# Optimization experiments

Measured on AMD Instinct MI355X. Metric: run time of the kernel, lower is better.

Reference implementation:

```python
import jax, jax.numpy as jnp
import numpy as np

N, E, G = 50000, 400000, 64          # nodes, edges, graphs in batch
IN_DIM, OUT_DIM = 64, 128
N_ETYPES, N_STEPS = 4, 8


def setup_inputs() -> dict:
    key = jax.random.key(0)
    ks = jax.random.split(key, 13)
    s = 1.0 / np.sqrt(OUT_DIM)
    u = lambda k, shp: jax.random.uniform(k, shp, jnp.float32, -s, s)
    return {
        "node_features": jax.random.normal(ks[0], (N, IN_DIM), jnp.float32),
        "src": jax.random.randint(ks[1], (E,), 0, N),
        "dst": jax.random.randint(ks[2], (E,), 0, N),
        "etype": jax.random.randint(ks[3], (E,), 0, N_ETYPES),
        "graph_ids": jax.random.randint(ks[4], (N,), 0, G),
        "Ws": u(ks[5], (N_ETYPES, OUT_DIM, OUT_DIM)),   # per-edge-type linear
        "bs": u(ks[6], (N_ETYPES, OUT_DIM)),
        "W_ih": u(ks[7], (3 * OUT_DIM, OUT_DIM)),        # GRUCell (r,z,n order)
        "W_hh": u(ks[8], (3 * OUT_DIM, OUT_DIM)),
        "b_ih": u(ks[9], (3 * OUT_DIM,)),
        "b_hh": u(ks[10], (3 * OUT_DIM,)),
        "W_cls": u(ks[11], (1, OUT_DIM + IN_DIM)),
        "b_cls": u(ks[12], (1,)),
    }


def _gru_cell(x, h, W_ih, W_hh, b_ih, b_hh):
    gi = x @ W_ih.T + b_ih
    gh = h @ W_hh.T + b_hh
    ir, iz, i_n = jnp.split(gi, 3, axis=-1)
    hr, hz, h_n = jnp.split(gh, 3, axis=-1)
    r = jax.nn.sigmoid(ir + hr)
    z = jax.nn.sigmoid(iz + hz)
    n = jnp.tanh(i_n + r * h_n)
    return (1.0 - z) * n + z * h


def reference(node_features, src, dst, etype, graph_ids,
              Ws, bs, W_ih, W_hh, b_ih, b_hh, W_cls, b_cls):
    # pad input features to OUT_DIM (GGNN.forward zero_pad)
    h = jnp.concatenate(
        [node_features, jnp.zeros((N, OUT_DIM - IN_DIM), node_features.dtype)], -1)

    def step(h, _):
        # per-edge-type linear transform of all node states: (T, N, D)
        Wh = jnp.einsum('nd,tkd->tnk', h, Ws) + bs[:, None, :]
        msg = Wh[etype, src]                                  # (E, D) gather
        a = jax.ops.segment_sum(msg, dst, num_segments=N)     # scatter-add
        return _gru_cell(a, h, W_ih, W_hh, b_ih, b_hh), None

    h, _ = jax.lax.scan(step, h, None, length=N_STEPS)

    hcat = jnp.concatenate([h, node_features], -1)            # (N, OUT+IN)
    feats = jax.ops.segment_sum(hcat, graph_ids, num_segments=G)  # sum readout
    return jax.nn.sigmoid(feats @ W_cls.T + b_cls)            # (G, 1)
```

## Files before the change

### kernel.cpp

```cpp
#include <hip/hip_runtime.h>
#include <hip/hip_bf16.h>
#include <math.h>


#define NN 50000
#define NE 400000
#define NG 64
#define IND 64
#define OD 128
#define LDO 896
#define RC 8

typedef _Float16 f16x8 __attribute__((ext_vector_type(8)));
typedef _Float16 f16x4 __attribute__((ext_vector_type(4)));
typedef _Float16 f16x2 __attribute__((ext_vector_type(2)));
typedef float f32x4 __attribute__((ext_vector_type(4)));

__device__ inline unsigned short f2h(float x) {
    _Float16 hv = (_Float16)x;
    unsigned short u;
    __builtin_memcpy(&u, &hv, 2);
    return u;
}

__global__ void k_cvt(const float* __restrict__ s, unsigned short* __restrict__ d, int n) {
    int i = blockIdx.x * 256 + threadIdx.x;
    if (i < n) d[i] = f2h(s[i]);
}

__global__ void k_init_h(const float* __restrict__ nf, float* __restrict__ h,
                         unsigned short* __restrict__ hb) {
    int i = blockIdx.x * 256 + threadIdx.x;
    if (i >= NN * OD) return;
    int n = i >> 7, d = i & 127;
    float v = (d < IND) ? nf[n * IND + d] : 0.f;
    h[i] = v;
    hb[i] = f2h(v);
}

__global__ void k_count(const int* __restrict__ dst, int* __restrict__ deg) {
    int e = blockIdx.x * 256 + threadIdx.x;
    if (e < NE) atomicAdd(&deg[dst[e]], 1);
}

__global__ void k_scan1(const int* __restrict__ deg, int* __restrict__ rowp,
                        int* __restrict__ bsum) {
    __shared__ int buf[1024];
    int tid = threadIdx.x;
    int i = blockIdx.x * 1024 + tid;
    int v = (i < NN) ? deg[i] : 0;
    buf[tid] = v;
    __syncthreads();
    for (int off = 1; off < 1024; off <<= 1) {
        int t = (tid >= off) ? buf[tid - off] : 0;
        __syncthreads();
        buf[tid] += t;
        __syncthreads();
    }
    if (i < NN) rowp[i + 1] = buf[tid];
    if (tid == 1023) bsum[blockIdx.x] = buf[tid];
}

__global__ void k_scan2(int* __restrict__ bsum, int nb) {
    __shared__ int buf[64];
    int tid = threadIdx.x;
    int v = (tid < nb) ? bsum[tid] : 0;
    buf[tid] = v;
    __syncthreads();
    for (int off = 1; off < 64; off <<= 1) {
        int t = (tid >= off) ? buf[tid - off] : 0;
        __syncthreads();
        buf[tid] += t;
        __syncthreads();
    }
    if (tid < nb) bsum[tid] = buf[tid] - v;
}

__global__ void k_scan3(const int* __restrict__ deg, const int* __restrict__ bsum,
                        int* __restrict__ rowp, int* __restrict__ cursor) {
    int i = blockIdx.x * 256 + threadIdx.x;
    if (i >= NN) return;
    int incl = rowp[i + 1] + bsum[i >> 10];
    rowp[i + 1] = incl;
    cursor[i] = incl - deg[i];
    if (i == 0) rowp[0] = 0;
}

__global__ void k_fill(const int* __restrict__ src, const int* __restrict__ dst,
                       const int* __restrict__ et, int* __restrict__ cursor,
                       int* __restrict__ ebase) {
    int e = blockIdx.x * 256 + threadIdx.x;
    if (e < NE) {
        int pos = atomicAdd(&cursor[dst[e]], 1);
        ebase[pos] = src[e] * LDO + et[e] * 128;
    }
}

__global__ void k_gcount(const int* __restrict__ gid, int* __restrict__ gdeg) {
    __shared__ int c[NG];
    int tid = threadIdx.x;
    if (tid < NG) c[tid] = 0;
    __syncthreads();
    int n = blockIdx.x * 1024 + tid;
    if (n < NN) atomicAdd(&c[gid[n]], 1);
    __syncthreads();
    if (tid < NG && c[tid] > 0) atomicAdd(&gdeg[tid], c[tid]);
}

__global__ void k_gscan(const int* __restrict__ gdeg, int* __restrict__ growp,
                        int* __restrict__ gcur) {
    __shared__ int buf[NG];
    int tid = threadIdx.x;
    int v = gdeg[tid];
    buf[tid] = v;
    __syncthreads();
    for (int off = 1; off < NG; off <<= 1) {
        int t = (tid >= off) ? buf[tid - off] : 0;
        __syncthreads();
        buf[tid] += t;
        __syncthreads();
    }
    growp[tid + 1] = buf[tid];
    gcur[tid] = buf[tid] - v;
    if (tid == 0) growp[0] = 0;
}

__global__ void k_gfill(const int* __restrict__ gid, int* __restrict__ gcur,
                        int* __restrict__ nlist) {
    __shared__ int lcnt[NG];
    __shared__ int lbase[NG];
    int tid = threadIdx.x;
    if (tid < NG) lcnt[tid] = 0;
    __syncthreads();
    int n = blockIdx.x * 1024 + tid;
    int g = -1, rank = 0;
    if (n < NN) { g = gid[n]; rank = atomicAdd(&lcnt[g], 1); }
    __syncthreads();
    if (tid < NG && lcnt[tid] > 0) lbase[tid] = atomicAdd(&gcur[tid], lcnt[tid]);
    __syncthreads();
    if (n < NN) nlist[lbase[g] + rank] = n;
}

__global__ __launch_bounds__(256) void k_gemm_mfma(
    const unsigned short* __restrict__ Ab, int M,
    const unsigned short* __restrict__ W0, const float* __restrict__ b0, int ngrp0,
    const unsigned short* __restrict__ W1, const float* __restrict__ b1,
    unsigned short* __restrict__ C) {
    __shared__ unsigned short As[128 * 136];
    __shared__ unsigned short Bs[128 * 136];

    const int g = blockIdx.y;
    const unsigned short* W;
    const float* bias;
    if (g < ngrp0) { W = W0 + (size_t)g * 16384; bias = b0 + g * 128; }
    else           { W = W1 + (size_t)(g - ngrp0) * 16384; bias = b1 + (g - ngrp0) * 128; }
    const int colbase = g * 128;
    const int m0 = blockIdx.x * 128;
    const int tid = threadIdx.x;

    const uint4* A4 = (const uint4*)Ab;
    const uint4* W4 = (const uint4*)W;

#pragma unroll
    for (int i = tid; i < 2048; i += 256) {
        int row = i >> 4, qq = i & 15;
        int n = m0 + row;
        uint4 va = (n < M) ? A4[(size_t)n * 16 + qq] : make_uint4(0u, 0u, 0u, 0u);
        *(uint4*)&As[row * 136 + qq * 8] = va;
        *(uint4*)&Bs[row * 136 + qq * 8] = W4[(size_t)row * 16 + qq];
    }
    __syncthreads();

    const int lane = tid & 63;
    const int w = tid >> 6;
    const int lr = lane & 15;
    const int q = lane >> 4;

    float bv[8];
#pragma unroll
    for (int nt = 0; nt < 8; ++nt) bv[nt] = bias[nt * 16 + lr];

    f32x4 acc[2][8];
#pragma unroll
    for (int mt = 0; mt < 2; ++mt)
#pragma unroll
        for (int nt = 0; nt < 8; ++nt) acc[mt][nt] = (f32x4){0.f, 0.f, 0.f, 0.f};

#pragma unroll
    for (int ks = 0; ks < 4; ++ks) {
        f16x8 af[2];
#pragma unroll
        for (int mt = 0; mt < 2; ++mt)
            af[mt] = *(const f16x8*)&As[(w * 32 + mt * 16 + lr) * 136 + ks * 32 + q * 8];
        f16x8 bfr[8];
#pragma unroll
        for (int nt = 0; nt < 8; ++nt)
            bfr[nt] = *(const f16x8*)&Bs[(nt * 16 + lr) * 136 + ks * 32 + q * 8];
#pragma unroll
        for (int mt = 0; mt < 2; ++mt)
#pragma unroll
            for (int nt = 0; nt < 8; ++nt)
                acc[mt][nt] = __builtin_amdgcn_mfma_f32_16x16x32_f16(
                    af[mt], bfr[nt], acc[mt][nt], 0, 0, 0);
    }

#pragma unroll
    for (int mt = 0; mt < 2; ++mt) {
        int rowbase = m0 + w * 32 + mt * 16 + q * 4;
#pragma unroll
        for (int r = 0; r < 4; ++r) {
            int n = rowbase + r;
            if (n < M) {
                unsigned short* crow = C + (size_t)n * LDO + colbase;
#pragma unroll
                for (int nt = 0; nt < 8; ++nt)
                    crow[nt * 16 + lr] = f2h(acc[mt][nt][r] + bv[nt]);
            }
        }
    }
}

__global__ void k_aggregate(const unsigned short* __restrict__ O,
                            const int* __restrict__ rowp, const int* __restrict__ ebase,
                            unsigned short* __restrict__ ab) {
    int wv = (blockIdx.x * 256 + threadIdx.x) >> 6;
    int lane = threadIdx.x & 63;
    int n = wv * 2 + (lane >> 5);
    if (n >= NN) return;
    int d4 = (lane & 31) * 4;
    int beg = rowp[n], end = rowp[n + 1];
    float a0 = 0.f, a1 = 0.f, a2 = 0.f, a3 = 0.f;
    for (int i = beg; i < end; ++i) {
        int b = ebase[i];
        f16x4 v = *(const f16x4*)&O[b + d4];
        a0 += (float)v[0]; a1 += (float)v[1]; a2 += (float)v[2]; a3 += (float)v[3];
    }
    f16x4 r;
    r[0] = (_Float16)a0; r[1] = (_Float16)a1; r[2] = (_Float16)a2; r[3] = (_Float16)a3;
    *(f16x4*)&ab[n * OD + d4] = r;
}

__global__ void k_gru(const unsigned short* __restrict__ O, float* __restrict__ h,
                      unsigned short* __restrict__ hb) {
    int i = blockIdx.x * 256 + threadIdx.x;
    if (i >= NN * 64) return;
    int n = i >> 6, p = (i & 63) * 2;
    const unsigned short* r = O + (size_t)n * LDO;
    f16x2 ir = *(const f16x2*)&r[p];
    f16x2 iz = *(const f16x2*)&r[128 + p];
    f16x2 in_ = *(const f16x2*)&r[256 + p];
    f16x2 hr = *(const f16x2*)&r[512 + p];
    f16x2 hz = *(const f16x2*)&r[640 + p];
    f16x2 hn = *(const f16x2*)&r[768 + p];
    float2 hv = *(const float2*)&h[(size_t)n * OD + p];
    float2 nh;
    {
        float rg = 1.f / (1.f + __expf(-((float)ir[0] + (float)hr[0])));
        float zg = 1.f / (1.f + __expf(-((float)iz[0] + (float)hz[0])));
        float ng = tanhf((float)in_[0] + rg * (float)hn[0]);
        nh.x = (1.f - zg) * ng + zg * hv.x;
        rg = 1.f / (1.f + __expf(-((float)ir[1] + (float)hr[1])));
        zg = 1.f / (1.f + __expf(-((float)iz[1] + (float)hz[1])));
        ng = tanhf((float)in_[1] + rg * (float)hn[1]);
        nh.y = (1.f - zg) * ng + zg * hv.y;
    }
    *(float2*)&h[(size_t)n * OD + p] = nh;
    f16x2 hb2; hb2[0] = (_Float16)nh.x; hb2[1] = (_Float16)nh.y;
    *(f16x2*)&hb[(size_t)n * OD + p] = hb2;
}

__global__ void k_readout(const float* __restrict__ h, const float* __restrict__ nf,
                          const int* __restrict__ nlist, const int* __restrict__ growp,
                          float* __restrict__ partial) {
    int g = blockIdx.x >> 3, c = blockIdx.x & (RC - 1);
    int d = threadIdx.x;
    int s = growp[g], e = growp[g + 1], len = e - s;
    int i0 = s + (int)((long long)len * c / RC);
    int i1 = s + (int)((long long)len * (c + 1) / RC);
    float acc = 0.f;
    for (int i = i0; i < i1; ++i) {
        int n = nlist[i];
        acc += (d < OD) ? h[(size_t)n * OD + d] : nf[(size_t)n * IND + (d - OD)];
    }
    partial[(size_t)blockIdx.x * 192 + d] = acc;
}

__global__ void k_reduce(const float* __restrict__ partial, float* __restrict__ feats) {
    int i = blockIdx.x * 256 + threadIdx.x;
    if (i >= NG * 192) return;
    int g = i / 192, d = i % 192;
    float s = 0.f;
    for (int c = 0; c < RC; ++c) s += partial[(size_t)(g * RC + c) * 192 + d];
    feats[i] = s;
}

__global__ void k_final(const float* __restrict__ feats, const float* __restrict__ W_cls,
                        const float* __restrict__ b_cls, float* __restrict__ out) {
    int g = threadIdx.x;
    if (g >= NG) return;
    float acc = b_cls[0];
    for (int d = 0; d < 192; ++d) acc += feats[g * 192 + d] * W_cls[d];
    out[g] = 1.f / (1.f + __expf(-acc));
}

extern "C" void kernel_launch(void* const* d_in, const int* in_sizes, int n_in,
                              void* d_out, int out_size, void* d_ws, size_t ws_size,
                              hipStream_t stream) {
    const float* nf    = (const float*)d_in[0];
    const int*   src   = (const int*)d_in[1];
    const int*   dst   = (const int*)d_in[2];
    const int*   et    = (const int*)d_in[3];
    const int*   gid   = (const int*)d_in[4];
    const float* Ws    = (const float*)d_in[5];
    const float* bs    = (const float*)d_in[6];
    const float* W_ih  = (const float*)d_in[7];
    const float* W_hh  = (const float*)d_in[8];
    const float* b_ih  = (const float*)d_in[9];
    const float* b_hh  = (const float*)d_in[10];
    const float* W_cls = (const float*)d_in[11];
    const float* b_cls = (const float*)d_in[12];
    float* out = (float*)d_out;

    char* ws = (char*)d_ws;
    size_t off = 0;
    auto alloc = [&](size_t bytes) -> void* {
        off = (off + 255) & ~(size_t)255;
        void* p = ws + off;
        off += bytes;
        return p;
    };
    float*          h    = (float*)alloc((size_t)NN * OD * 4);
    unsigned short* O    = (unsigned short*)alloc((size_t)NN * LDO * 2);
    unsigned short* hb   = (unsigned short*)alloc((size_t)NN * OD * 2);
    unsigned short* ab   = (unsigned short*)alloc((size_t)NN * OD * 2);
    int*   deg    = (int*)alloc((size_t)NN * 4);
    int*   rowp   = (int*)alloc((size_t)(NN + 1) * 4);
    int*   cursor = (int*)alloc((size_t)NN * 4);
    int*   ebase  = (int*)alloc((size_t)NE * 4);
    int*   bsum   = (int*)alloc(64 * 4);
    int*   gdeg   = (int*)alloc(NG * 4);
    int*   growp  = (int*)alloc((NG + 1) * 4);
    int*   gcur   = (int*)alloc(NG * 4);
    int*   nlist  = (int*)alloc((size_t)NN * 4);
    float* feats  = (float*)alloc((size_t)NG * 192 * 4);
    unsigned short* wsb  = (unsigned short*)alloc((size_t)4 * 16384 * 2);
    unsigned short* wihb = (unsigned short*)alloc((size_t)3 * 16384 * 2);
    unsigned short* whhb = (unsigned short*)alloc((size_t)3 * 16384 * 2);
    (void)ws_size; (void)in_sizes; (void)n_in; (void)out_size;

    float* partial = (float*)O;

    hipMemsetAsync(deg, 0, (size_t)NN * 4, stream);
    hipMemsetAsync(gdeg, 0, NG * 4, stream);

    k_cvt<<<(4 * 16384 + 255) / 256, 256, 0, stream>>>(Ws, wsb, 4 * 16384);
    k_cvt<<<(3 * 16384 + 255) / 256, 256, 0, stream>>>(W_ih, wihb, 3 * 16384);
    k_cvt<<<(3 * 16384 + 255) / 256, 256, 0, stream>>>(W_hh, whhb, 3 * 16384);

    k_init_h<<<(NN * OD + 255) / 256, 256, 0, stream>>>(nf, h, hb);
    k_count<<<(NE + 255) / 256, 256, 0, stream>>>(dst, deg);
    const int nb = (NN + 1023) / 1024;
    k_scan1<<<nb, 1024, 0, stream>>>(deg, rowp, bsum);
    k_scan2<<<1, 64, 0, stream>>>(bsum, nb);
    k_scan3<<<(NN + 255) / 256, 256, 0, stream>>>(deg, bsum, rowp, cursor);
    k_fill<<<(NE + 255) / 256, 256, 0, stream>>>(src, dst, et, cursor, ebase);

    k_gcount<<<nb, 1024, 0, stream>>>(gid, gdeg);
    k_gscan<<<1, NG, 0, stream>>>(gdeg, growp, gcur);
    k_gfill<<<nb, 1024, 0, stream>>>(gid, gcur, nlist);

    const int mt = (NN + 127) / 128;
    const int aggblk = (NN * 32 + 255) / 256;
    for (int s = 0; s < 8; ++s) {
        k_gemm_mfma<<<dim3(mt, 7), 256, 0, stream>>>(hb, NN, wsb, bs, 4, whhb, b_hh, O);
        k_aggregate<<<aggblk, 256, 0, stream>>>(O, rowp, ebase, ab);
        k_gemm_mfma<<<dim3(mt, 3), 256, 0, stream>>>(ab, NN, wihb, b_ih, 3, wihb, b_ih, O);
        k_gru<<<(NN * 64 + 255) / 256, 256, 0, stream>>>(O, h, hb);
    }

    k_readout<<<NG * RC, 192, 0, stream>>>(h, nf, nlist, growp, partial);
    k_reduce<<<(NG * 192 + 255) / 256, 256, 0, stream>>>(partial, feats);
    k_final<<<1, 64, 0, stream>>>(feats, W_cls, b_cls, out);
}
```

Measured before the change: 1.102 ms.

## Fuse GRU input/hidden GEMMs with gate math into one MFMA kernel

Replaces the separate W_hh GEMM (formerly appended to the edge-type GEMM), the W_ih GEMM and the elementwise GRU kernel with a single k_gates kernel. That kernel computes both gate projections with MFMA per 64-node tile and applies the sigmoid and tanh gates in registers. This removes writing the 6x128 gate pre-activations to the O buffer and reading them back, and drops one launch per step; O shrinks to 512 columns. In exchange, each block reloads the gate weights into LDS for each of the three gates and writes h with less coalesced scalar stores.

```diff
diff --git a/kernel.cpp b/kernel.cpp
--- a/kernel.cpp
+++ b/kernel.cpp
@@ -8,7 +8,7 @@
 #define NG 64
 #define IND 64
 #define OD 128
-#define LDO 896
+#define LDO 512
 #define RC 8
 
 typedef _Float16 f16x8 __attribute__((ext_vector_type(8)));
@@ -22,6 +22,7 @@
     __builtin_memcpy(&u, &hv, 2);
     return u;
 }
+__device__ inline float sigf(float x) { return 1.f / (1.f + __expf(-x)); }
 
 __global__ void k_cvt(const float* __restrict__ s, unsigned short* __restrict__ d, int n) {
     int i = blockIdx.x * 256 + threadIdx.x;
@@ -143,17 +144,14 @@
 
 __global__ __launch_bounds__(256) void k_gemm_mfma(
     const unsigned short* __restrict__ Ab, int M,
-    const unsigned short* __restrict__ W0, const float* __restrict__ b0, int ngrp0,
-    const unsigned short* __restrict__ W1, const float* __restrict__ b1,
+    const unsigned short* __restrict__ W0, const float* __restrict__ b0,
     unsigned short* __restrict__ C) {
     __shared__ unsigned short As[128 * 136];
     __shared__ unsigned short Bs[128 * 136];
 
     const int g = blockIdx.y;
-    const unsigned short* W;
-    const float* bias;
-    if (g < ngrp0) { W = W0 + (size_t)g * 16384; bias = b0 + g * 128; }
-    else           { W = W1 + (size_t)(g - ngrp0) * 16384; bias = b1 + (g - ngrp0) * 128; }
+    const unsigned short* W = W0 + (size_t)g * 16384;
+    const float* bias = b0 + g * 128;
     const int colbase = g * 128;
     const int m0 = blockIdx.x * 128;
     const int tid = threadIdx.x;
@@ -240,33 +238,100 @@
     *(f16x4*)&ab[n * OD + d4] = r;
 }
 
-__global__ void k_gru(const unsigned short* __restrict__ O, float* __restrict__ h,
-                      unsigned short* __restrict__ hb) {
-    int i = blockIdx.x * 256 + threadIdx.x;
-    if (i >= NN * 64) return;
-    int n = i >> 6, p = (i & 63) * 2;
-    const unsigned short* r = O + (size_t)n * LDO;
-    f16x2 ir = *(const f16x2*)&r[p];
-    f16x2 iz = *(const f16x2*)&r[128 + p];
-    f16x2 in_ = *(const f16x2*)&r[256 + p];
-    f16x2 hr = *(const f16x2*)&r[512 + p];
-    f16x2 hz = *(const f16x2*)&r[640 + p];
-    f16x2 hn = *(const f16x2*)&r[768 + p];
-    float2 hv = *(const float2*)&h[(size_t)n * OD + p];
-    float2 nh;
-    {
-        float rg = 1.f / (1.f + __expf(-((float)ir[0] + (float)hr[0])));
-        float zg = 1.f / (1.f + __expf(-((float)iz[0] + (float)hz[0])));
-        float ng = tanhf((float)in_[0] + rg * (float)hn[0]);
-        nh.x = (1.f - zg) * ng + zg * hv.x;
-        rg = 1.f / (1.f + __expf(-((float)ir[1] + (float)hr[1])));
-        zg = 1.f / (1.f + __expf(-((float)iz[1] + (float)hz[1])));
-        ng = tanhf((float)in_[1] + rg * (float)hn[1]);
-        nh.y = (1.f - zg) * ng + zg * hv.y;
-    }
-    *(float2*)&h[(size_t)n * OD + p] = nh;
-    f16x2 hb2; hb2[0] = (_Float16)nh.x; hb2[1] = (_Float16)nh.y;
-    *(f16x2*)&hb[(size_t)n * OD + p] = hb2;
+__global__ __launch_bounds__(256) void k_gates(
+    const unsigned short* __restrict__ ab, const unsigned short* __restrict__ hbin,
+    const unsigned short* __restrict__ Wi, const unsigned short* __restrict__ Wh,
+    const float* __restrict__ b_ih, const float* __restrict__ b_hh,
+    float* __restrict__ h, unsigned short* __restrict__ hbout) {
+    __shared__ unsigned short Wis[128 * 136];
+    __shared__ unsigned short Whs[128 * 136];
+
+    const int n0 = blockIdx.x * 64;
+    const int tid = threadIdx.x;
+    const int lane = tid & 63;
+    const int w = tid >> 6;
+    const int lr = lane & 15;
+    const int q = lane >> 4;
+    const int arow = n0 + w * 16 + lr;
+    const bool rok = arow < NN;
+
+    const uint4* Wi4 = (const uint4*)Wi;
+    const uint4* Wh4 = (const uint4*)Wh;
+
+    f16x8 zf;
+#pragma unroll
+    for (int j = 0; j < 8; ++j) zf[j] = (_Float16)0.f;
+
+    f32x4 rg[8], zg[8];
+
+    for (int g = 0; g < 3; ++g) {
+        __syncthreads();
+#pragma unroll
+        for (int i = tid; i < 2048; i += 256) {
+            int row = i >> 4, qq = i & 15;
+            *(uint4*)&Wis[row * 136 + qq * 8] = Wi4[(size_t)(g * 128 + row) * 16 + qq];
+            *(uint4*)&Whs[row * 136 + qq * 8] = Wh4[(size_t)(g * 128 + row) * 16 + qq];
+        }
+        __syncthreads();
+
+        f16x8 af_a[4], af_h[4];
+#pragma unroll
+        for (int ks = 0; ks < 4; ++ks) {
+            af_a[ks] = rok ? *(const f16x8*)&ab[(size_t)arow * OD + ks * 32 + q * 8] : zf;
+            af_h[ks] = rok ? *(const f16x8*)&hbin[(size_t)arow * OD + ks * 32 + q * 8] : zf;
+        }
+
+        f32x4 ai[8], ah[8];
+#pragma unroll
+        for (int nt = 0; nt < 8; ++nt) { ai[nt] = (f32x4){0.f,0.f,0.f,0.f}; ah[nt] = (f32x4){0.f,0.f,0.f,0.f}; }
+
+#pragma unroll
+        for (int ks = 0; ks < 4; ++ks) {
+            f16x8 bfr[8];
+#pragma unroll
+            for (int nt = 0; nt < 8; ++nt)
+                bfr[nt] = *(const f16x8*)&Wis[(nt * 16 + lr) * 136 + ks * 32 + q * 8];
+#pragma unroll
+            for (int nt = 0; nt < 8; ++nt)
+                ai[nt] = __builtin_amdgcn_mfma_f32_16x16x32_f16(af_a[ks], bfr[nt], ai[nt], 0, 0, 0);
+#pragma unroll
+            for (int nt = 0; nt < 8; ++nt)
+                bfr[nt] = *(const f16x8*)&Whs[(nt * 16 + lr) * 136 + ks * 32 + q * 8];
+#pragma unroll
+            for (int nt = 0; nt < 8; ++nt)
+                ah[nt] = __builtin_amdgcn_mfma_f32_16x16x32_f16(af_h[ks], bfr[nt], ah[nt], 0, 0, 0);
+        }
+
+        if (g < 2) {
+#pragma unroll
+            for (int nt = 0; nt < 8; ++nt) {
+                int d = nt * 16 + lr;
+                float bi = b_ih[g * 128 + d], bh = b_hh[g * 128 + d];
+#pragma unroll
+                for (int r = 0; r < 4; ++r) {
+                    float v = sigf(ai[nt][r] + bi + ah[nt][r] + bh);
+                    if (g == 0) rg[nt][r] = v; else zg[nt][r] = v;
+                }
+            }
+        } else {
+#pragma unroll
+            for (int nt = 0; nt < 8; ++nt) {
+                int d = nt * 16 + lr;
+                float bi = b_ih[256 + d], bh = b_hh[256 + d];
+#pragma unroll
+                for (int r = 0; r < 4; ++r) {
+                    int orow = n0 + w * 16 + q * 4 + r;
+                    if (orow < NN) {
+                        float ng = tanhf(ai[nt][r] + bi + rg[nt][r] * (ah[nt][r] + bh));
+                        float hv = h[(size_t)orow * OD + d];
+                        float nh = (1.f - zg[nt][r]) * ng + zg[nt][r] * hv;
+                        h[(size_t)orow * OD + d] = nh;
+                        hbout[(size_t)orow * OD + d] = f2h(nh);
+                    }
+                }
+            }
+        }
+    }
 }
 
 __global__ void k_readout(const float* __restrict__ h, const float* __restrict__ nf,
@@ -371,11 +436,11 @@
 
     const int mt = (NN + 127) / 128;
     const int aggblk = (NN * 32 + 255) / 256;
+    const int gateblk = (NN + 63) / 64;
     for (int s = 0; s < 8; ++s) {
-        k_gemm_mfma<<<dim3(mt, 7), 256, 0, stream>>>(hb, NN, wsb, bs, 4, whhb, b_hh, O);
+        k_gemm_mfma<<<dim3(mt, 4), 256, 0, stream>>>(hb, NN, wsb, bs, O);
         k_aggregate<<<aggblk, 256, 0, stream>>>(O, rowp, ebase, ab);
-        k_gemm_mfma<<<dim3(mt, 3), 256, 0, stream>>>(ab, NN, wihb, b_ih, 3, wihb, b_ih, O);
-        k_gru<<<(NN * 64 + 255) / 256, 256, 0, stream>>>(O, h, hb);
+        k_gates<<<gateblk, 256, 0, stream>>>(ab, hb, wihb, whhb, b_ih, b_hh, h, hb);
     }
 
     k_readout<<<NG * RC, 192, 0, stream>>>(h, nf, nlist, growp, partial);
```

Measured after the change: 1.547 ms. 1.4x slower.

## Fold edge-type weights into GRU input weights and aggregate raw h per type

Applied to the files above, without the earlier changes.

Precomputes W_ih·Ws per edge type into one combined weight matrix and folds the per-type biases via per-node type-degree counts. Each step now aggregates raw fp16 h into four per-type sums, then runs a single GEMM with K=640 that yields the r/z gates already summed plus the separate input and hidden n parts. This drops the wide per-type transform of all nodes and its 896-wide intermediate, and goes from two GEMMs plus aggregate plus GRU to three kernels per step. In exchange the aggregation keeps four accumulator sets and writes 4x wider rows, the fp16 rounding order changes, and one-time setup kernels are added.

```diff
diff --git a/kernel.cpp b/kernel.cpp
--- a/kernel.cpp
+++ b/kernel.cpp
@@ -8,12 +8,12 @@
 #define NG 64
 #define IND 64
 #define OD 128
-#define LDO 896
+#define LDX 640
+#define LDP 512
 #define RC 8
 
 typedef _Float16 f16x8 __attribute__((ext_vector_type(8)));
 typedef _Float16 f16x4 __attribute__((ext_vector_type(4)));
-typedef _Float16 f16x2 __attribute__((ext_vector_type(2)));
 typedef float f32x4 __attribute__((ext_vector_type(4)));
 
 __device__ inline unsigned short f2h(float x) {
@@ -22,25 +22,69 @@
     __builtin_memcpy(&u, &hv, 2);
     return u;
 }
-
-__global__ void k_cvt(const float* __restrict__ s, unsigned short* __restrict__ d, int n) {
-    int i = blockIdx.x * 256 + threadIdx.x;
-    if (i < n) d[i] = f2h(s[i]);
-}
+__device__ inline float sigf(float x) { return 1.f / (1.f + __expf(-x)); }
 
 __global__ void k_init_h(const float* __restrict__ nf, float* __restrict__ h,
-                         unsigned short* __restrict__ hb) {
+                         unsigned short* __restrict__ x) {
     int i = blockIdx.x * 256 + threadIdx.x;
     if (i >= NN * OD) return;
     int n = i >> 7, d = i & 127;
     float v = (d < IND) ? nf[n * IND + d] : 0.f;
     h[i] = v;
-    hb[i] = f2h(v);
-}
-
-__global__ void k_count(const int* __restrict__ dst, int* __restrict__ deg) {
+    x[(size_t)n * LDX + 512 + d] = f2h(v);
+}
+
+__global__ void k_wbig(const float* __restrict__ Ws, const float* __restrict__ W_ih,
+                       const float* __restrict__ W_hh, unsigned short* __restrict__ Wbig) {
+    int o2 = blockIdx.x;
+    for (int c = threadIdx.x; c < LDX; c += 256) {
+        float v = 0.f;
+        if (c < 512) {
+            if (o2 < 384) {
+                int t = c >> 7, k = c & 127;
+                const float* wi = W_ih + (size_t)o2 * 128;
+                const float* ws = Ws + (size_t)t * 16384 + k;
+                float acc = 0.f;
+                for (int o = 0; o < 128; ++o) acc += wi[o] * ws[(size_t)o * 128];
+                v = acc;
+            }
+        } else {
+            int k = c - 512;
+            if (o2 < 256)      v = W_hh[(size_t)o2 * 128 + k];
+            else if (o2 >= 384) v = W_hh[(size_t)(o2 - 384 + 256) * 128 + k];
+        }
+        Wbig[(size_t)o2 * LDX + c] = f2h(v);
+    }
+}
+
+__global__ void k_wbias(const float* __restrict__ W_ih, const float* __restrict__ bs,
+                        const float* __restrict__ b_ih, const float* __restrict__ b_hh,
+                        float* __restrict__ bias512, float* __restrict__ dbv) {
+    int o2 = threadIdx.x;
+    float b;
+    if (o2 < 256)      b = b_ih[o2] + b_hh[o2];
+    else if (o2 < 384) b = b_ih[o2];
+    else               b = b_hh[o2 - 384 + 256];
+    bias512[o2] = b;
+    for (int t = 0; t < 4; ++t) {
+        float acc = 0.f;
+        if (o2 < 384) {
+            const float* wi = W_ih + (size_t)o2 * 128;
+            const float* bt = bs + t * 128;
+            for (int k = 0; k < 128; ++k) acc += wi[k] * bt[k];
+        }
+        dbv[o2 * 4 + t] = acc;
+    }
+}
+
+__global__ void k_count4(const int* __restrict__ dst, const int* __restrict__ et,
+                         int* __restrict__ deg, int* __restrict__ deg4) {
     int e = blockIdx.x * 256 + threadIdx.x;
-    if (e < NE) atomicAdd(&deg[dst[e]], 1);
+    if (e < NE) {
+        int d = dst[e];
+        atomicAdd(&deg[d], 1);
+        atomicAdd(&deg4[d * 4 + et[e]], 1);
+    }
 }
 
 __global__ void k_scan1(const int* __restrict__ deg, int* __restrict__ rowp,
@@ -88,11 +132,11 @@
 
 __global__ void k_fill(const int* __restrict__ src, const int* __restrict__ dst,
                        const int* __restrict__ et, int* __restrict__ cursor,
-                       int* __restrict__ ebase) {
+                       int* __restrict__ epack) {
     int e = blockIdx.x * 256 + threadIdx.x;
     if (e < NE) {
         int pos = atomicAdd(&cursor[dst[e]], 1);
-        ebase[pos] = src[e] * LDO + et[e] * 128;
+        epack[pos] = src[e] * 4 + et[e];
     }
 }
 
@@ -141,132 +185,140 @@
     if (n < NN) nlist[lbase[g] + rank] = n;
 }
 
-__global__ __launch_bounds__(256) void k_gemm_mfma(
-    const unsigned short* __restrict__ Ab, int M,
-    const unsigned short* __restrict__ W0, const float* __restrict__ b0, int ngrp0,
-    const unsigned short* __restrict__ W1, const float* __restrict__ b1,
-    unsigned short* __restrict__ C) {
-    __shared__ unsigned short As[128 * 136];
-    __shared__ unsigned short Bs[128 * 136];
-
-    const int g = blockIdx.y;
-    const unsigned short* W;
-    const float* bias;
-    if (g < ngrp0) { W = W0 + (size_t)g * 16384; bias = b0 + g * 128; }
-    else           { W = W1 + (size_t)(g - ngrp0) * 16384; bias = b1 + (g - ngrp0) * 128; }
-    const int colbase = g * 128;
-    const int m0 = blockIdx.x * 128;
-    const int tid = threadIdx.x;
-
-    const uint4* A4 = (const uint4*)Ab;
-    const uint4* W4 = (const uint4*)W;
-
-#pragma unroll
-    for (int i = tid; i < 2048; i += 256) {
-        int row = i >> 4, qq = i & 15;
-        int n = m0 + row;
-        uint4 va = (n < M) ? A4[(size_t)n * 16 + qq] : make_uint4(0u, 0u, 0u, 0u);
-        *(uint4*)&As[row * 136 + qq * 8] = va;
-        *(uint4*)&Bs[row * 136 + qq * 8] = W4[(size_t)row * 16 + qq];
-    }
-    __syncthreads();
-
-    const int lane = tid & 63;
-    const int w = tid >> 6;
-    const int lr = lane & 15;
-    const int q = lane >> 4;
-
-    float bv[8];
-#pragma unroll
-    for (int nt = 0; nt < 8; ++nt) bv[nt] = bias[nt * 16 + lr];
-
-    f32x4 acc[2][8];
-#pragma unroll
-    for (int mt = 0; mt < 2; ++mt)
-#pragma unroll
-        for (int nt = 0; nt < 8; ++nt) acc[mt][nt] = (f32x4){0.f, 0.f, 0.f, 0.f};
-
-#pragma unroll
-    for (int ks = 0; ks < 4; ++ks) {
-        f16x8 af[2];
-#pragma unroll
-        for (int mt = 0; mt < 2; ++mt)
-            af[mt] = *(const f16x8*)&As[(w * 32 + mt * 16 + lr) * 136 + ks * 32 + q * 8];
-        f16x8 bfr[8];
-#pragma unroll
-        for (int nt = 0; nt < 8; ++nt)
-            bfr[nt] = *(const f16x8*)&Bs[(nt * 16 + lr) * 136 + ks * 32 + q * 8];
-#pragma unroll
-        for (int mt = 0; mt < 2; ++mt)
-#pragma unroll
-            for (int nt = 0; nt < 8; ++nt)
-                acc[mt][nt] = __builtin_amdgcn_mfma_f32_16x16x32_f16(
-                    af[mt], bfr[nt], acc[mt][nt], 0, 0, 0);
-    }
-
-#pragma unroll
-    for (int mt = 0; mt < 2; ++mt) {
-        int rowbase = m0 + w * 32 + mt * 16 + q * 4;
-#pragma unroll
-        for (int r = 0; r < 4; ++r) {
-            int n = rowbase + r;
-            if (n < M) {
-                unsigned short* crow = C + (size_t)n * LDO + colbase;
-#pragma unroll
-                for (int nt = 0; nt < 8; ++nt)
-                    crow[nt * 16 + lr] = f2h(acc[mt][nt][r] + bv[nt]);
-            }
-        }
-    }
-}
-
-__global__ void k_aggregate(const unsigned short* __restrict__ O,
-                            const int* __restrict__ rowp, const int* __restrict__ ebase,
-                            unsigned short* __restrict__ ab) {
+__global__ void k_agg4(unsigned short* x, const int* __restrict__ rowp,
+                       const int* __restrict__ epack) {
     int wv = (blockIdx.x * 256 + threadIdx.x) >> 6;
     int lane = threadIdx.x & 63;
     int n = wv * 2 + (lane >> 5);
     if (n >= NN) return;
     int d4 = (lane & 31) * 4;
     int beg = rowp[n], end = rowp[n + 1];
-    float a0 = 0.f, a1 = 0.f, a2 = 0.f, a3 = 0.f;
+    float acc[4][4];
+#pragma unroll
+    for (int t = 0; t < 4; ++t)
+#pragma unroll
+        for (int j = 0; j < 4; ++j) acc[t][j] = 0.f;
     for (int i = beg; i < end; ++i) {
-        int b = ebase[i];
-        f16x4 v = *(const f16x4*)&O[b + d4];
-        a0 += (float)v[0]; a1 += (float)v[1]; a2 += (float)v[2]; a3 += (float)v[3];
-    }
-    f16x4 r;
-    r[0] = (_Float16)a0; r[1] = (_Float16)a1; r[2] = (_Float16)a2; r[3] = (_Float16)a3;
-    *(f16x4*)&ab[n * OD + d4] = r;
-}
-
-__global__ void k_gru(const unsigned short* __restrict__ O, float* __restrict__ h,
-                      unsigned short* __restrict__ hb) {
+        int p = epack[i];
+        int t = p & 3;
+        f16x4 v = *(const f16x4*)&x[(size_t)(p >> 2) * LDX + 512 + d4];
+        float v0 = (float)v[0], v1 = (float)v[1], v2 = (float)v[2], v3 = (float)v[3];
+        if (t == 0)      { acc[0][0] += v0; acc[0][1] += v1; acc[0][2] += v2; acc[0][3] += v3; }
+        else if (t == 1) { acc[1][0] += v0; acc[1][1] += v1; acc[1][2] += v2; acc[1][3] += v3; }
+        else if (t == 2) { acc[2][0] += v0; acc[2][1] += v1; acc[2][2] += v2; acc[2][3] += v3; }
+        else             { acc[3][0] += v0; acc[3][1] += v1; acc[3][2] += v2; acc[3][3] += v3; }
+    }
+#pragma unroll
+    for (int t = 0; t < 4; ++t) {
+        f16x4 r;
+        r[0] = (_Float16)acc[t][0]; r[1] = (_Float16)acc[t][1];
+        r[2] = (_Float16)acc[t][2]; r[3] = (_Float16)acc[t][3];
+        *(f16x4*)&x[(size_t)n * LDX + t * 128 + d4] = r;
+    }
+}
+
+__global__ __launch_bounds__(256) void k_gpre(
+    const unsigned short* __restrict__ x, const unsigned short* __restrict__ Wbig,
+    const float* __restrict__ bias512, const float* __restrict__ dbv,
+    const int* __restrict__ deg4, unsigned short* __restrict__ P) {
+    __shared__ unsigned short As[128 * 136];
+    __shared__ unsigned short Bs[128 * 136];
+
+    const int g = blockIdx.y;
+    const int m0 = blockIdx.x * 128;
+    const int tid = threadIdx.x;
+
+    const uint4* A4 = (const uint4*)x;
+    const uint4* W4 = (const uint4*)Wbig;
+
+    const int lane = tid & 63;
+    const int w = tid >> 6;
+    const int lr = lane & 15;
+    const int q = lane >> 4;
+
+    f32x4 acc[2][8];
+#pragma unroll
+    for (int mt = 0; mt < 2; ++mt)
+#pragma unroll
+        for (int nt = 0; nt < 8; ++nt) acc[mt][nt] = (f32x4){0.f, 0.f, 0.f, 0.f};
+
+    for (int c = 0; c < 5; ++c) {
+#pragma unroll
+        for (int i = tid; i < 2048; i += 256) {
+            int row = i >> 4, qq = i & 15;
+            int n = m0 + row;
+            uint4 va = (n < NN) ? A4[(size_t)n * 80 + c * 16 + qq] : make_uint4(0u, 0u, 0u, 0u);
+            *(uint4*)&As[row * 136 + qq * 8] = va;
+            *(uint4*)&Bs[row * 136 + qq * 8] = W4[(size_t)(g * 128 + row) * 80 + c * 16 + qq];
+        }
+        __syncthreads();
+#pragma unroll
+        for (int ks = 0; ks < 4; ++ks) {
+            f16x8 af[2];
+#pragma unroll
+            for (int mt = 0; mt < 2; ++mt)
+                af[mt] = *(const f16x8*)&As[(w * 32 + mt * 16 + lr) * 136 + ks * 32 + q * 8];
+            f16x8 bfr[8];
+#pragma unroll
+            for (int nt = 0; nt < 8; ++nt)
+                bfr[nt] = *(const f16x8*)&Bs[(nt * 16 + lr) * 136 + ks * 32 + q * 8];
+#pragma unroll
+            for (int mt = 0; mt < 2; ++mt)
+#pragma unroll
+                for (int nt = 0; nt < 8; ++nt)
+                    acc[mt][nt] = __builtin_amdgcn_mfma_f32_16x16x32_f16(
+                        af[mt], bfr[nt], acc[mt][nt], 0, 0, 0);
+        }
+        __syncthreads();
+    }
+
+#pragma unroll
+    for (int mt = 0; mt < 2; ++mt) {
+        int rowbase = m0 + w * 32 + mt * 16 + q * 4;
+#pragma unroll
+        for (int r = 0; r < 4; ++r) {
+            int n = rowbase + r;
+            if (n < NN) {
+                int4 dg = *(const int4*)&deg4[n * 4];
+                unsigned short* prow = P + (size_t)n * LDP + g * 128;
+#pragma unroll
+                for (int nt = 0; nt < 8; ++nt) {
+                    int o = g * 128 + nt * 16 + lr;
+                    float v = acc[mt][nt][r] + bias512[o]
+                            + (float)dg.x * dbv[o * 4 + 0] + (float)dg.y * dbv[o * 4 + 1]
+                            + (float)dg.z * dbv[o * 4 + 2] + (float)dg.w * dbv[o * 4 + 3];
+                    prow[nt * 16 + lr] = f2h(v);
+                }
+            }
+        }
+    }
+}
+
+__global__ void k_gru2(const unsigned short* __restrict__ P, float* __restrict__ h,
+                       unsigned short* x) {
     int i = blockIdx.x * 256 + threadIdx.x;
-    if (i >= NN * 64) return;
-    int n = i >> 6, p = (i & 63) * 2;
-    const unsigned short* r = O + (size_t)n * LDO;
-    f16x2 ir = *(const f16x2*)&r[p];
-    f16x2 iz = *(const f16x2*)&r[128 + p];
-    f16x2 in_ = *(const f16x2*)&r[256 + p];
-    f16x2 hr = *(const f16x2*)&r[512 + p];
-    f16x2 hz = *(const f16x2*)&r[640 + p];
-    f16x2 hn = *(const f16x2*)&r[768 + p];
-    float2 hv = *(const float2*)&h[(size_t)n * OD + p];
-    float2 nh;
-    {
-        float rg = 1.f / (1.f + __expf(-((float)ir[0] + (float)hr[0])));
-        float zg = 1.f / (1.f + __expf(-((float)iz[0] + (float)hz[0])));
-        float ng = tanhf((float)in_[0] + rg * (float)hn[0]);
-        nh.x = (1.f - zg) * ng + zg * hv.x;
-        rg = 1.f / (1.f + __expf(-((float)ir[1] + (float)hr[1])));
-        zg = 1.f / (1.f + __expf(-((float)iz[1] + (float)hz[1])));
-        ng = tanhf((float)in_[1] + rg * (float)hn[1]);
-        nh.y = (1.f - zg) * ng + zg * hv.y;
-    }
-    *(float2*)&h[(size_t)n * OD + p] = nh;
-    f16x2 hb2; hb2[0] = (_Float16)nh.x; hb2[1] = (_Float16)nh.y;
-    *(f16x2*)&hb[(size_t)n * OD + p] = hb2;
+    if (i >= NN * 32) return;
+    int n = i >> 5, d = (i & 31) * 4;
+    const unsigned short* pr = P + (size_t)n * LDP;
+    f16x4 vr = *(const f16x4*)&pr[d];
+    f16x4 vz = *(const f16x4*)&pr[128 + d];
+    f16x4 vi = *(const f16x4*)&pr[256 + d];
+    f16x4 vh = *(const f16x4*)&pr[384 + d];
+    float4 hv = *(const float4*)&h[(size_t)n * OD + d];
+    float nh[4];
+    float hvv[4] = {hv.x, hv.y, hv.z, hv.w};
+#pragma unroll
+    for (int j = 0; j < 4; ++j) {
+        float r = sigf((float)vr[j]);
+        float z = sigf((float)vz[j]);
+        float ng = tanhf((float)vi[j] + r * (float)vh[j]);
+        nh[j] = (1.f - z) * ng + z * hvv[j];
+    }
+    *(float4*)&h[(size_t)n * OD + d] = make_float4(nh[0], nh[1], nh[2], nh[3]);
+    f16x4 hb4;
+    hb4[0] = (_Float16)nh[0]; hb4[1] = (_Float16)nh[1];
+    hb4[2] = (_Float16)nh[2]; hb4[3] = (_Float16)nh[3];
+    *(f16x4*)&x[(size_t)n * LDX + 512 + d] = hb4;
 }
 
 __global__ void k_readout(const float* __restrict__ h, const float* __restrict__ nf,
@@ -329,41 +381,41 @@
         off += bytes;
         return p;
     };
-    float*          h    = (float*)alloc((size_t)NN * OD * 4);
-    unsigned short* O    = (unsigned short*)alloc((size_t)NN * LDO * 2);
-    unsigned short* hb   = (unsigned short*)alloc((size_t)NN * OD * 2);
-    unsigned short* ab   = (unsigned short*)alloc((size_t)NN * OD * 2);
+    float*          h     = (float*)alloc((size_t)NN * OD * 4);
+    unsigned short* x     = (unsigned short*)alloc((size_t)NN * LDX * 2);
+    unsigned short* P     = (unsigned short*)alloc((size_t)NN * LDP * 2);
+    unsigned short* Wbig  = (unsigned short*)alloc((size_t)512 * LDX * 2);
+    float* bias512 = (float*)alloc(512 * 4);
+    float* dbv     = (float*)alloc(512 * 4 * 4);
     int*   deg    = (int*)alloc((size_t)NN * 4);
+    int*   deg4   = (int*)alloc((size_t)NN * 4 * 4);
     int*   rowp   = (int*)alloc((size_t)(NN + 1) * 4);
     int*   cursor = (int*)alloc((size_t)NN * 4);
-    int*   ebase  = (int*)alloc((size_t)NE * 4);
+    int*   epack  = (int*)alloc((size_t)NE * 4);
     int*   bsum   = (int*)alloc(64 * 4);
     int*   gdeg   = (int*)alloc(NG * 4);
     int*   growp  = (int*)alloc((NG + 1) * 4);
     int*   gcur   = (int*)alloc(NG * 4);
     int*   nlist  = (int*)alloc((size_t)NN * 4);
     float* feats  = (float*)alloc((size_t)NG * 192 * 4);
-    unsigned short* wsb  = (unsigned short*)alloc((size_t)4 * 16384 * 2);
-    unsigned short* wihb = (unsigned short*)alloc((size_t)3 * 16384 * 2);
-    unsigned short* whhb = (unsigned short*)alloc((size_t)3 * 16384 * 2);
     (void)ws_size; (void)in_sizes; (void)n_in; (void)out_size;
 
-    float* partial = (float*)O;
+    float* partial = (float*)P;
 
     hipMemsetAsync(deg, 0, (size_t)NN * 4, stream);
+    hipMemsetAsync(deg4, 0, (size_t)NN * 4 * 4, stream);
     hipMemsetAsync(gdeg, 0, NG * 4, stream);
 
-    k_cvt<<<(4 * 16384 + 255) / 256, 256, 0, stream>>>(Ws, wsb, 4 * 16384);
-    k_cvt<<<(3 * 16384 + 255) / 256, 256, 0, stream>>>(W_ih, wihb, 3 * 16384);
-    k_cvt<<<(3 * 16384 + 255) / 256, 256, 0, stream>>>(W_hh, whhb, 3 * 16384);
-
-    k_init_h<<<(NN * OD + 255) / 256, 256, 0, stream>>>(nf, h, hb);
-    k_count<<<(NE + 255) / 256, 256, 0, stream>>>(dst, deg);
+    k_wbig<<<512, 256, 0, stream>>>(Ws, W_ih, W_hh, Wbig);
+    k_wbias<<<1, 512, 0, stream>>>(W_ih, bs, b_ih, b_hh, bias512, dbv);
+
+    k_init_h<<<(NN * OD + 255) / 256, 256, 0, stream>>>(nf, h, x);
+    k_count4<<<(NE + 255) / 256, 256, 0, stream>>>(dst, et, deg, deg4);
     const int nb = (NN + 1023) / 1024;
     k_scan1<<<nb, 1024, 0, stream>>>(deg, rowp, bsum);
     k_scan2<<<1, 64, 0, stream>>>(bsum, nb);
     k_scan3<<<(NN + 255) / 256, 256, 0, stream>>>(deg, bsum, rowp, cursor);
-    k_fill<<<(NE + 255) / 256, 256, 0, stream>>>(src, dst, et, cursor, ebase);
+    k_fill<<<(NE + 255) / 256, 256, 0, stream>>>(src, dst, et, cursor, epack);
 
     k_gcount<<<nb, 1024, 0, stream>>>(gid, gdeg);
     k_gscan<<<1, NG, 0, stream>>>(gdeg, growp, gcur);
@@ -372,10 +424,9 @@
     const int mt = (NN + 127) / 128;
     const int aggblk = (NN * 32 + 255) / 256;
     for (int s = 0; s < 8; ++s) {
-        k_gemm_mfma<<<dim3(mt, 7), 256, 0, stream>>>(hb, NN, wsb, bs, 4, whhb, b_hh, O);
-        k_aggregate<<<aggblk, 256, 0, stream>>>(O, rowp, ebase, ab);
-        k_gemm_mfma<<<dim3(mt, 3), 256, 0, stream>>>(ab, NN, wihb, b_ih, 3, wihb, b_ih, O);
-        k_gru<<<(NN * 64 + 255) / 256, 256, 0, stream>>>(O, h, hb);
+        k_agg4<<<aggblk, 256, 0, stream>>>(x, rowp, epack);
+        k_gpre<<<dim3(mt, 4), 256, 0, stream>>>(x, Wbig, bias512, dbv, deg4, P);
+        k_gru2<<<(NN * 32 + 255) / 256, 256, 0, stream>>>(P, h, x);
     }
 
     k_readout<<<NG * RC, 192, 0, stream>>>(h, nf, nlist, growp, partial);
```

Measured after the change: 1.473 ms. +33.7%, slower.
